# Kernel optimization log

Measured on AMD Instinct MI355X. Metric: run time of the kernel, lower is better.

Reference implementation:

```python
import jax, jax.numpy as jnp
import numpy as np

B, S, D = 8, 1024, 768          # batch, block_size, d_model
H = 6                            # n_head
E = 24                           # n_experts
CAP = 4                          # n_expert_capacity
DH = D // H                      # 128, head dim
DF = 384                         # d_ffn
N = S * H                        # tokens after head split = 6144
K = N * CAP // E                 # tokens per expert = 1024


def _uniform(key, shape, fan_in):
    b = 1.0 / np.sqrt(fan_in)
    return jax.random.uniform(key, shape, jnp.float32, -b, b)


def setup_inputs() -> dict:
    key = jax.random.key(0)
    kx, kc, k1, k2, kh, km = jax.random.split(key, 6)
    return {
        "x": jax.random.normal(kx, (B, S, D), jnp.float32),
        "choice": _uniform(kc, (E, DH), DH),
        "w1": _uniform(k1, (E, DH, DF), DH),
        "w2": _uniform(k2, (E, DF, DH), DF),
        "head": _uniform(kh, (D, D), D),
        "merge": _uniform(km, (D, D), D),
    }


def reference(x, choice, w1, w2, head, merge):
    Bb = x.shape[0]
    # input projection then split heads into a token stream of length N
    x = jnp.einsum("bsd,do->bso", x, head)
    x = x.reshape(Bb, N, DH)                              # [B, N, DH]
    # expert-choice routing: softmax over experts per token
    gates = jax.nn.softmax(jnp.einsum("bsd,ed->bse", x, choice), axis=-1)
    # each expert picks its top-K tokens
    G, I = jax.lax.top_k(jnp.swapaxes(gates, -1, -2), K)  # [B, E, K]
    bidx = jnp.arange(Bb)[:, None, None]
    # gather (equivalent to one-hot matmul einsum('beks,bsd->bekd', P, x))
    x_in = x[bidx, I]                                     # [B, E, K, DH]
    # per-expert SwiGLU-free FFN: silu(x w1) w2
    h = jax.nn.silu(jnp.einsum("bekd,edo->beko", x_in, w1))
    x_mlp = jnp.einsum("beki,eid->bekd", h, w2)           # [B, E, K, DH]
    # scatter-combine weighted by gates (einsum('beks,bek,bekd->bsd'))
    x_out = jnp.zeros((Bb, N, DH), x.dtype).at[bidx, I].add(G[..., None] * x_mlp)
    # dropout is identity in eval mode
    x_out = x_out.reshape(Bb, S, D)
    return jnp.einsum("bsd,do->bso", x_out, merge)
```

## Files before the change

kernel.cpp:

```cpp
#include <hip/hip_runtime.h>
#include <stdint.h>
#include <math.h>

typedef __attribute__((ext_vector_type(8))) short short8;
typedef __attribute__((ext_vector_type(4))) short short4v;
typedef __attribute__((ext_vector_type(4))) float floatx4;
typedef __attribute__((ext_vector_type(2))) float floatx2;
typedef __attribute__((ext_vector_type(4))) double double4v;

#define DEV static __device__ __forceinline__

DEV float bf2f(unsigned short u){ union { unsigned int i; float f; } c; c.i = ((unsigned int)u) << 16; return c.f; }
DEV unsigned short f2bf(float f){ union { float f; unsigned int i; } c; c.f = f; unsigned int u = c.i; u += 0x7fffu + ((u >> 16) & 1u); return (unsigned short)(u >> 16); }

#if defined(__has_builtin)
#if __has_builtin(__builtin_amdgcn_global_load_lds)
#define USE_GLL 1
#endif
#if __has_builtin(__builtin_amdgcn_exp2f) && __has_builtin(__builtin_amdgcn_rcpf)
#define FAST_SILU 1
#endif
#endif
#ifndef USE_GLL
#define USE_GLL 0
#endif
#ifndef FAST_SILU
#define FAST_SILU 0
#endif

DEV void gll16(const unsigned short* g, unsigned short* ldsbase, int lane){
#if USE_GLL
  __builtin_amdgcn_global_load_lds((const __attribute__((address_space(1))) void*)g,
                                   (__attribute__((address_space(3))) void*)ldsbase, 16, 0, 0);
#else
  *(short8*)(ldsbase + lane * 8) = *(const short8*)g;
#endif
}

DEV float silu(float v){
#if FAST_SILU
  float ex = __builtin_amdgcn_exp2f(v * -1.44269504088896f);
  return v * __builtin_amdgcn_rcpf(1.f + ex);
#else
  return v / (1.f + __expf(-v));
#endif
}

DEV void transpose_tile(const float* in, unsigned short* out, int R, int C,
                        int bx, int by, int bz, int tid, unsigned short* tile)
{
  const long boff = (long)bz * (long)R * (long)C;
  in += boff; out += boff;
  const int c0 = bx * 64, r0 = by * 64;
  const int rr = tid >> 4;
  const int c4 = (tid & 15) * 4;
#pragma unroll
  for (int i = 0; i < 4; i++){
    int r = rr + i * 16;
    floatx4 v = *(const floatx4*)(in + (long)(r0 + r) * C + c0 + c4);
#pragma unroll
    for (int u = 0; u < 4; u++) tile[r * 68 + c4 + u] = f2bf(v[u]);
  }
  __syncthreads();
#pragma unroll
  for (int i = 0; i < 4; i++){
    int cc = rr + i * 16;
    short4v v;
#pragma unroll
    for (int u = 0; u < 4; u++) v[u] = (short)tile[(c4 + u) * 68 + cc];
    *(short4v*)(out + (long)(c0 + cc) * R + r0 + c4) = v;
  }
}

__global__ __launch_bounds__(256) void k_prep(const float* __restrict__ x,
    const float* __restrict__ choice, const float* __restrict__ w1,
    const float* __restrict__ w2, const float* __restrict__ head,
    const float* __restrict__ merge,
    unsigned short* __restrict__ xb, unsigned short* __restrict__ headT,
    unsigned short* __restrict__ mergeT, unsigned short* __restrict__ w1T,
    unsigned short* __restrict__ w2T, double* __restrict__ W64,
    unsigned int* __restrict__ probe)
{
  __shared__ double buf[1536];
  unsigned short* tile = (unsigned short*)buf;
  const int id = blockIdx.x, tid = threadIdx.x;
  if (id < 144){
    transpose_tile(head, headT, 768, 768, id % 12, id / 12, 0, tid, tile);
  } else if (id < 288){
    int l = id - 144;
    transpose_tile(merge, mergeT, 768, 768, l % 12, l / 12, 0, tid, tile);
  } else if (id < 576){
    int l = id - 288;
    transpose_tile(w1, w1T, 128, 384, l % 6, (l / 6) % 2, l / 12, tid, tile);
  } else if (id < 864){
    int l = id - 576;
    transpose_tile(w2, w2T, 384, 128, l % 2, (l / 2) % 6, l / 12, tid, tile);
  } else if (id < 1248){
    int l = id - 864;
    const int sub = tid >> 7, lt = tid & 127;
    const int d = l * 2 + sub;
    double* hrow = buf + sub * 768;
    for (int i = lt; i < 768; i += 128) hrow[i] = (double)head[(long)d * 768 + i];
    __syncthreads();
    for (int c = lt; c < 144; c += 128){
      int h = c / 24, e = c % 24;
      double a = 0.0;
      const double* hr = hrow + h * 128;
      const float* ch = choice + e * 128;
#pragma unroll 8
      for (int k = 0; k < 128; k++) a += hr[k] * (double)ch[k];
      W64[(long)d * 144 + c] = a;
    }
  } else if (id < 7392){
    const long l = id - 1248;
    const long i = (l * 256 + tid) * 4;
    floatx4 v = *(const floatx4*)(x + i);
    short4v o;
#pragma unroll
    for (int u = 0; u < 4; u++) o[u] = (short)f2bf(v[u]);
    *(short4v*)(xb + i) = o;
  } else {
    if (tid < 64){
      double4v z = {0.0, 0.0, 0.0, 0.0};
      double4v d1 = __builtin_amdgcn_mfma_f64_16x16x4f64((double)tid, 1.0, z, 0, 0, 0);
      double4v d2 = __builtin_amdgcn_mfma_f64_16x16x4f64(1.0, (double)tid, z, 0, 0, 0);
      const int V0 = (int)d1[0];
      const int Astd = ((V0 & 3) == 0) ? 1 : 0;
      unsigned int rp = 0;
      int V;
      V = (int)d1[0]; rp |= (unsigned int)(Astd ? (V - 96) >> 2 : (V - 6) >> 4);
      V = (int)d1[1]; rp |= (unsigned int)(Astd ? (V - 96) >> 2 : (V - 6) >> 4) << 8;
      V = (int)d1[2]; rp |= (unsigned int)(Astd ? (V - 96) >> 2 : (V - 6) >> 4) << 16;
      V = (int)d1[3]; rp |= (unsigned int)(Astd ? (V - 96) >> 2 : (V - 6) >> 4) << 24;
      const int W0 = (int)d2[0];
      const int Bstd = ((W0 & 3) == 0) ? 1 : 0;
      const int cl = Bstd ? (W0 - 96) >> 2 : (W0 - 6) >> 4;
      probe[tid] = rp;
      probe[64 + tid] = (unsigned int)cl;
      if (tid == 0) probe[128] = (unsigned int)(Astd | (Bstd << 1));
    }
  }
}

template<int OUTF>
DEV void gemm_body(const unsigned short* __restrict__ A, const unsigned short* __restrict__ BT,
                   unsigned short* __restrict__ C, float* __restrict__ Cf, int N, int K,
                   unsigned short* As, unsigned short* Bs, int m0, int n0, int tid)
{
  const int lane = tid & 63;
  const int w = tid >> 6;
  const int wy = w >> 1, wx = w & 1;

  floatx4 acc[4][4];
  {
    floatx4 z4 = {0.f, 0.f, 0.f, 0.f};
#pragma unroll
    for (int i = 0; i < 4; i++)
#pragma unroll
      for (int j = 0; j < 4; j++) acc[i][j] = z4;
  }

  const int rsub = lane >> 3;
  const int kcol = (lane & 7) * 8;

  for (int k0 = 0; k0 < K; k0 += 64){
#pragma unroll
    for (int i = 0; i < 4; i++){
      const int inst = w * 4 + i;
      const int rr = inst * 8 + rsub;
      gll16(A + (long)(m0 + rr) * K + k0 + kcol, &As[inst * 512], lane);
      gll16(BT + (long)(n0 + rr) * K + k0 + kcol, &Bs[inst * 512], lane);
    }
    __syncthreads();
#pragma unroll
    for (int ks = 0; ks < 2; ++ks){
      const int kb = ks * 32 + (lane >> 4) * 8;
      short8 af[4], bfr[4];
#pragma unroll
      for (int mi = 0; mi < 4; mi++) af[mi]  = *(const short8*)&As[(wy * 64 + mi * 16 + (lane & 15)) * 64 + kb];
#pragma unroll
      for (int ni = 0; ni < 4; ni++) bfr[ni] = *(const short8*)&Bs[(wx * 64 + ni * 16 + (lane & 15)) * 64 + kb];
#pragma unroll
      for (int mi = 0; mi < 4; mi++)
#pragma unroll
        for (int ni = 0; ni < 4; ni++)
          acc[mi][ni] = __builtin_amdgcn_mfma_f32_16x16x32_bf16(af[mi], bfr[ni], acc[mi][ni], 0, 0, 0);
    }
    __syncthreads();
  }

  const int ml = lane & 15;
  const int rq = (lane >> 4) * 4;
#pragma unroll
  for (int mi = 0; mi < 4; mi++){
    const int rowb = m0 + wy * 64 + mi * 16 + rq;
#pragma unroll
    for (int ni = 0; ni < 4; ni++){
      const int col = n0 + wx * 64 + ni * 16 + ml;
#pragma unroll
      for (int r = 0; r < 4; r++){
        float v = acc[mi][ni][r];
        if (OUTF) Cf[(long)(rowb + r) * N + col] = v;
        else      C[(long)(rowb + r) * N + col] = f2bf(v);
      }
    }
  }
}

DEV void gates_mfma(const float* __restrict__ xg, const double* __restrict__ W,
                    double* __restrict__ P, const unsigned int* __restrict__ probe,
                    int id, int tid)
{
  const int lane = tid & 63, w = tid >> 6;
  const unsigned int flags = probe[128];
  const int Astd = (int)(flags & 1u), Bstd = (int)((flags >> 1) & 1u);
  const unsigned int rp = probe[lane];
  const int cl = (int)probe[64 + lane];
  const int ar = Astd ? (lane & 15) : (lane >> 2);
  const int ak = Astd ? (lane >> 4) : (lane & 3);
  const int bk = Bstd ? (lane >> 4) : (lane & 3);
  const int bj = Bstd ? (lane & 15) : (lane >> 2);

  const int kseg = id >> 7;
  const int row0 = (id & 127) * 64 + w * 16;

  double4v acc[9];
#pragma unroll
  for (int t = 0; t < 9; t++) acc[t] = (double4v){0.0, 0.0, 0.0, 0.0};

  const float* arow = xg + (long)(row0 + ar) * 768;
  const int kbase = kseg * 192;
  for (int kc = 0; kc < 192; kc += 4){
    const int k0 = kbase + kc;
    const double a = (double)arow[k0 + ak];
    const double* wr = W + (long)(k0 + bk) * 144 + bj;
#pragma unroll
    for (int t = 0; t < 9; t++)
      acc[t] = __builtin_amdgcn_mfma_f64_16x16x4f64(a, wr[t * 16], acc[t], 0, 0, 0);
  }

  const int r0_ = (int)(rp & 255u), r1_ = (int)((rp >> 8) & 255u);
  const int r2_ = (int)((rp >> 16) & 255u), r3_ = (int)((rp >> 24) & 255u);
  double* dst = P + (long)kseg * 8192 * 144 + (long)row0 * 144;
#pragma unroll
  for (int t = 0; t < 9; t++){
    const int cb = t * 16 + cl;
    dst[(long)r0_ * 144 + cb] = acc[t][0];
    dst[(long)r1_ * 144 + cb] = acc[t][1];
    dst[(long)r2_ * 144 + cb] = acc[t][2];
    dst[(long)r3_ * 144 + cb] = acc[t][3];
  }
}

__global__ __launch_bounds__(256, 4) void k_main0(const unsigned short* __restrict__ xb,
    const unsigned short* __restrict__ headT, unsigned short* __restrict__ x1,
    const float* __restrict__ xg, const double* __restrict__ W, double* __restrict__ P,
    const unsigned int* __restrict__ probe)
{
  __shared__ unsigned short lds[128 * 64 * 2];
  const int id = blockIdx.x, tid = threadIdx.x;
  if (id < 512){
    gates_mfma(xg, W, P, probe, id, tid);
  } else {
    const int id2 = id - 512;
    unsigned short* As = lds;
    unsigned short* Bs = As + 128 * 64;
    gemm_body<0>(xb, headT, x1, nullptr, 768, 768, As, Bs, (id2 & 63) * 128, (id2 >> 6) * 128, tid);
  }
}

__global__ __launch_bounds__(256) void k_softmax(const double* __restrict__ P,
                                                 double* __restrict__ gatesT)
{
  const int gid = blockIdx.x * 256 + threadIdx.x;
  const int R = gid / 6, h = gid % 6;
  const int b = R >> 10, s = R & 1023;
  const int n = s * 6 + h;
  const long S = (long)8192 * 144;
  const long base = (long)R * 144 + h * 24;
  double l[24];
#pragma unroll
  for (int e = 0; e < 24; e++){
    const long o = base + e;
    l[e] = (P[o] + P[S + o]) + (P[2 * S + o] + P[3 * S + o]);
  }
  double m = l[0];
#pragma unroll
  for (int e = 1; e < 24; e++) m = fmax(m, l[e]);
  double ssum = 0.0;
#pragma unroll
  for (int e = 0; e < 24; e++){ l[e] = exp(l[e] - m); ssum += l[e]; }
  double is = 1.0 / ssum;
#pragma unroll
  for (int e = 0; e < 24; e++)
    gatesT[((long)(b * 24 + e)) * 6144 + n] = l[e] * is;
}

DEV int blk_reduce(int v, volatile int* sbuf, int tid){
#pragma unroll
  for (int off = 32; off > 0; off >>= 1) v += __shfl_down(v, off);
  __syncthreads();
  if ((tid & 63) == 0) sbuf[tid >> 6] = v;
  __syncthreads();
  return sbuf[0] + sbuf[1] + sbuf[2] + sbuf[3];
}

__global__ __launch_bounds__(256) void k_topk(const double* __restrict__ gatesT,
                                              int* __restrict__ Kidx, float* __restrict__ Gval,
                                              int* __restrict__ cnt, unsigned short* __restrict__ inv)
{
  __shared__ int sbuf[4];
  __shared__ int s_pos;
  __shared__ unsigned long long mm[8];
  const int tid = threadIdx.x;
  const int be = blockIdx.x;
  const int b = be / 24, e = be % 24;
  const double* g = gatesT + (long)be * 6144;

  unsigned long long key[24];
#pragma unroll
  for (int j = 0; j < 24; j++)
    key[j] = (unsigned long long)__double_as_longlong(g[tid + 256 * j]);

  unsigned long long mn = key[0], mx = key[0];
#pragma unroll
  for (int j = 1; j < 24; j++){
    mn = key[j] < mn ? key[j] : mn;
    mx = key[j] > mx ? key[j] : mx;
  }
#pragma unroll
  for (int off = 32; off > 0; off >>= 1){
    unsigned long long a = (unsigned long long)__shfl_down((long long)mn, off);
    unsigned long long c = (unsigned long long)__shfl_down((long long)mx, off);
    mn = a < mn ? a : mn;
    mx = c > mx ? c : mx;
  }
  if ((tid & 63) == 0){ mm[(tid >> 6) * 2] = mn; mm[(tid >> 6) * 2 + 1] = mx; }
  __syncthreads();
  mn = mm[0]; mx = mm[1];
#pragma unroll
  for (int q = 1; q < 4; q++){
    mn = mm[2 * q] < mn ? mm[2 * q] : mn;
    mx = mm[2 * q + 1] > mx ? mm[2 * q + 1] : mx;
  }

  unsigned long long lo = mn - 1ull, hi = mx;
  for (int it = 0; it < 64; ++it){
    if (hi - lo <= 1ull) break;
    unsigned long long mid = lo + ((hi - lo) >> 1);
    int c = 0;
#pragma unroll
    for (int j = 0; j < 24; j++) c += (key[j] > mid) ? 1 : 0;
    c = blk_reduce(c, sbuf, tid);
    if (c >= 1024) lo = mid; else hi = mid;
  }
  const unsigned long long T = hi;
  int cg = 0;
#pragma unroll
  for (int j = 0; j < 24; j++) cg += (key[j] > T) ? 1 : 0;
  cg = blk_reduce(cg, sbuf, tid);
  const int need = 1024 - cg;

  int lo2 = 0, hi2 = 6144;
  for (int it = 0; it < 13; ++it){
    if (hi2 - lo2 <= 1) break;
    int mid = (lo2 + hi2) >> 1;
    int c = 0;
#pragma unroll
    for (int j = 0; j < 24; j++) c += (key[j] == T && (tid + 256 * j) < mid) ? 1 : 0;
    c = blk_reduce(c, sbuf, tid);
    if (c >= need) hi2 = mid; else lo2 = mid;
  }
  const int m = hi2;

  if (tid == 0) s_pos = 0;
  __syncthreads();
#pragma unroll
  for (int j = 0; j < 24; j++){
    int n = tid + 256 * j;
    bool sel = (key[j] > T) || (key[j] == T && n < m);
    if (sel){
      int slot = atomicAdd(&s_pos, 1);
      Kidx[(long)be * 1024 + slot] = n;
      Gval[(long)be * 1024 + slot] = (float)__longlong_as_double((long long)key[j]);
      int t = b * 6144 + n;
      int p = atomicAdd(&cnt[t], 1);
      inv[(long)t * 24 + p] = (unsigned short)(e * 1024 + slot);
    }
  }
}

__global__ __launch_bounds__(256, 2) void k_gemm2(const unsigned short* __restrict__ A,
    const unsigned short* __restrict__ BT, float* __restrict__ Cf)
{
  __shared__ unsigned short As[128 * 64];
  __shared__ unsigned short Bs[128 * 64];
  gemm_body<1>(A, BT, nullptr, Cf, 768, 768, As, Bs,
               (int)blockIdx.x * 128, (int)blockIdx.y * 128, (int)threadIdx.x);
}

__global__ __launch_bounds__(256, 4) void k_ffn(const unsigned short* __restrict__ x1,
    const unsigned short* __restrict__ w1T, const unsigned short* __restrict__ w2T,
    const int* __restrict__ KidxAll, const float* __restrict__ GvalAll,
    unsigned short* __restrict__ Y)
{
  __shared__ unsigned short W1c[64 * 128];
  __shared__ unsigned short W2c[128 * 64];
  __shared__ unsigned short Hc[64 * 64];
  const int tid = threadIdx.x, lane = tid & 63, w = tid >> 6;
  const int tx = lane & 15, quad = lane >> 4;
  const int mt = blockIdx.x;
  const int be = blockIdx.y;
  const int b = be / 24, e = be % 24;
  const int* idx = KidxAll + (long)be * 1024 + mt * 64;
  const float* scl = GvalAll + (long)be * 1024 + mt * 64;
  const unsigned short* A   = x1  + (long)b * 6144 * 128;
  const unsigned short* w1e = w1T + (long)e * 384 * 128;
  const unsigned short* w2e = w2T + (long)e * 128 * 384;

  short8 afr[4];
  {
    const int r0 = idx[w * 16 + tx];
    const unsigned short* a0 = A + (long)r0 * 128 + quad * 8;
#pragma unroll
    for (int ks = 0; ks < 4; ks++) afr[ks] = *(const short8*)(a0 + ks * 32);
  }

  floatx4 Yt[2][4];
  {
    floatx4 z4 = {0.f, 0.f, 0.f, 0.f};
#pragma unroll
    for (int i = 0; i < 2; i++)
#pragma unroll
      for (int j = 0; j < 4; j++) Yt[i][j] = z4;
  }

  for (int nc = 0; nc < 6; ++nc){
    {
      const int r0 = w * 16;
#pragma unroll
      for (int i = 0; i < 4; i++){
        int lr = r0 + i * 4 + quad;
        int c = tx ^ (lr & 15);
        gll16(w1e + (long)(nc * 64 + lr) * 128 + c * 8, &W1c[(r0 + i * 4) * 128], lane);
      }
    }
    {
      const int r0 = w * 32;
#pragma unroll
      for (int i = 0; i < 4; i++){
        int rr = r0 + i * 8 + (lane >> 3);
        int c = (lane & 7) ^ (rr & 7);
        gll16(w2e + (long)rr * 384 + nc * 64 + c * 8, &W2c[(r0 + i * 8) * 64], lane);
      }
    }
    __syncthreads();

    floatx4 h4[4];
    {
      floatx4 z4 = {0.f, 0.f, 0.f, 0.f};
#pragma unroll
      for (int j = 0; j < 4; j++) h4[j] = z4;
    }
#pragma unroll
    for (int ks = 0; ks < 4; ++ks){
      const int chunk = ks * 4 + quad;
      const int pos = chunk ^ tx;
#pragma unroll
      for (int nf = 0; nf < 4; ++nf){
        short8 bfr = *(const short8*)&W1c[(nf * 16 + tx) * 128 + pos * 8];
        h4[nf] = __builtin_amdgcn_mfma_f32_16x16x32_bf16(afr[ks], bfr, h4[nf], 0, 0, 0);
      }
    }
#pragma unroll
    for (int nf = 0; nf < 4; ++nf){
      const int hchunk = nf * 2 + (tx >> 3);
      const int hoff = tx & 7;
#pragma unroll
      for (int r = 0; r < 4; r++){
        float v = silu(h4[nf][r]);
        const int trow = w * 16 + quad * 4 + r;
        Hc[trow * 64 + (hchunk ^ (trow & 7)) * 8 + hoff] = f2bf(v);
      }
    }
    __syncthreads();

#pragma unroll
    for (int ks = 0; ks < 2; ++ks){
      const int chunk2 = ks * 4 + quad;
      const int posx = chunk2 ^ (tx & 7);
      short8 a2[2], b2[4];
#pragma unroll
      for (int mf = 0; mf < 2; ++mf)
        a2[mf] = *(const short8*)&W2c[(w * 32 + mf * 16 + tx) * 64 + posx * 8];
#pragma unroll
      for (int nf = 0; nf < 4; ++nf)
        b2[nf] = *(const short8*)&Hc[(nf * 16 + tx) * 64 + posx * 8];
#pragma unroll
      for (int mf = 0; mf < 2; ++mf)
#pragma unroll
        for (int nf = 0; nf < 4; ++nf)
          Yt[mf][nf] = __builtin_amdgcn_mfma_f32_16x16x32_bf16(a2[mf], b2[nf], Yt[mf][nf], 0, 0, 0);
    }
    __syncthreads();
  }

#pragma unroll
  for (int nf = 0; nf < 4; ++nf){
    const int rb = nf * 16 + tx;
    const float g = scl[rb];
    unsigned short* dst = Y + ((long)be * 1024 + mt * 64 + rb) * 128 + w * 32 + quad * 4;
#pragma unroll
    for (int mf = 0; mf < 2; ++mf){
      short4v v;
#pragma unroll
      for (int r = 0; r < 4; r++) v[r] = (short)f2bf(Yt[mf][nf][r] * g);
      *(short4v*)(dst + mf * 16) = v;
    }
  }
}

__global__ __launch_bounds__(256) void k_combine(const int* __restrict__ cnt,
    const unsigned short* __restrict__ inv, const unsigned short* __restrict__ Y,
    unsigned short* __restrict__ xout)
{
  const int t = blockIdx.x * 4 + (threadIdx.x >> 6);
  const int lane = threadIdx.x & 63;
  const int b = t / 6144;
  const int c = cnt[t];
  float a0 = 0.f, a1 = 0.f;
  for (int p = 0; p < c; ++p){
    int code = inv[(long)t * 24 + p];
    int e = code >> 10, slot = code & 1023;
    const unsigned short* y = Y + (((long)(b * 24 + e) * 1024 + slot) << 7) + lane * 2;
    a0 += bf2f(y[0]); a1 += bf2f(y[1]);
  }
  unsigned short* o = xout + ((long)t << 7) + lane * 2;
  o[0] = f2bf(a0); o[1] = f2bf(a1);
}

extern "C" void kernel_launch(void* const* d_in, const int* in_sizes, int n_in,
                              void* d_out, int out_size, void* d_ws, size_t ws_size,
                              hipStream_t stream)
{
  const float* x      = (const float*)d_in[0];
  const float* choice = (const float*)d_in[1];
  const float* w1     = (const float*)d_in[2];
  const float* w2     = (const float*)d_in[3];
  const float* head   = (const float*)d_in[4];
  const float* merge  = (const float*)d_in[5];
  float* out = (float*)d_out;
  (void)in_sizes; (void)n_in; (void)out_size; (void)ws_size;

  char* p = (char*)d_ws;
  auto alloc = [&p](size_t bytes) -> void* {
    void* q = (void*)p; p += (bytes + 255) & ~(size_t)255; return q;
  };

  unsigned short* headT = (unsigned short*)alloc((size_t)768 * 768 * 2);
  unsigned short* mergeT= (unsigned short*)alloc((size_t)768 * 768 * 2);
  unsigned short* w1T   = (unsigned short*)alloc((size_t)24 * 384 * 128 * 2);
  unsigned short* w2T   = (unsigned short*)alloc((size_t)24 * 128 * 384 * 2);
  double* W64           = (double*)alloc((size_t)768 * 144 * 8);
  int* Kidx             = (int*)alloc((size_t)192 * 1024 * 4);
  float* Gval           = (float*)alloc((size_t)192 * 1024 * 4);
  int* cnt              = (int*)alloc((size_t)49152 * 4);
  unsigned short* inv   = (unsigned short*)alloc((size_t)49152 * 24 * 2);
  unsigned short* xb    = (unsigned short*)alloc((size_t)8192 * 768 * 2);
  unsigned short* x1    = (unsigned short*)alloc((size_t)8192 * 768 * 2);
  unsigned short* Y     = (unsigned short*)alloc((size_t)192 * 1024 * 128 * 2);
  double* P             = (double*)Y;
  double* gatesT        = (double*)((char*)Y + (size_t)4 * 8192 * 144 * 8);
  unsigned short* xout  = xb;
  unsigned int* probe   = (unsigned int*)Kidx;

  hipMemsetAsync(cnt, 0, (size_t)49152 * 4, stream);
  k_prep<<<dim3(7393), 256, 0, stream>>>(x, choice, w1, w2, head, merge,
                                         xb, headT, mergeT, w1T, w2T, W64, probe);
  k_main0<<<dim3(896), 256, 0, stream>>>(xb, headT, x1, x, W64, P, probe);
  k_softmax<<<dim3(192), 256, 0, stream>>>(P, gatesT);
  k_topk<<<dim3(192), 256, 0, stream>>>(gatesT, Kidx, Gval, cnt, inv);
  k_ffn<<<dim3(16, 192, 1), 256, 0, stream>>>(x1, w1T, w2T, Kidx, Gval, Y);
  k_combine<<<dim3(12288), 256, 0, stream>>>(cnt, inv, Y, xout);
  k_gemm2<<<dim3(64, 6, 1), 256, 0, stream>>>(xout, mergeT, out);
}
```

Baseline: 335.6 us.

## Halve gate k-split, single-barrier topk reduction, batch combine gathers

Gate-logit MFMA work is split into two k-segments of 384 instead of four of 192, so fewer partial buffers are written and summed in softmax. The block reduction in top-k uses a double-buffered shared array so each step needs one barrier instead of two. The combine kernel loads four inverse-index codes at once and issues four independent 32-bit gathers per iteration to raise memory-level parallelism. The gates split trades parallelism (fewer blocks, longer per-block loops) for less partial-sum traffic.

```diff
diff --git a/kernel.cpp b/kernel.cpp
--- a/kernel.cpp
+++ b/kernel.cpp
@@ -229,8 +229,8 @@
   for (int t = 0; t < 9; t++) acc[t] = (double4v){0.0, 0.0, 0.0, 0.0};
 
   const float* arow = xg + (long)(row0 + ar) * 768;
-  const int kbase = kseg * 192;
-  for (int kc = 0; kc < 192; kc += 4){
+  const int kbase = kseg * 384;
+  for (int kc = 0; kc < 384; kc += 4){
     const int k0 = kbase + kc;
     const double a = (double)arow[k0 + ak];
     const double* wr = W + (long)(k0 + bk) * 144 + bj;
@@ -259,10 +259,10 @@
 {
   __shared__ unsigned short lds[128 * 64 * 2];
   const int id = blockIdx.x, tid = threadIdx.x;
-  if (id < 512){
+  if (id < 256){
     gates_mfma(xg, W, P, probe, id, tid);
   } else {
-    const int id2 = id - 512;
+    const int id2 = id - 256;
     unsigned short* As = lds;
     unsigned short* Bs = As + 128 * 64;
     gemm_body<0>(xb, headT, x1, nullptr, 768, 768, As, Bs, (id2 & 63) * 128, (id2 >> 6) * 128, tid);
@@ -282,7 +282,7 @@
 #pragma unroll
   for (int e = 0; e < 24; e++){
     const long o = base + e;
-    l[e] = (P[o] + P[S + o]) + (P[2 * S + o] + P[3 * S + o]);
+    l[e] = P[o] + P[S + o];
   }
   double m = l[0];
 #pragma unroll
@@ -296,26 +296,27 @@
     gatesT[((long)(b * 24 + e)) * 6144 + n] = l[e] * is;
 }
 
-DEV int blk_reduce(int v, volatile int* sbuf, int tid){
+DEV int blk_reduce(int v, volatile int* sbuf, int tid, int ph){
 #pragma unroll
   for (int off = 32; off > 0; off >>= 1) v += __shfl_down(v, off);
+  volatile int* sb = sbuf + (ph & 1) * 4;
+  if ((tid & 63) == 0) sb[tid >> 6] = v;
   __syncthreads();
-  if ((tid & 63) == 0) sbuf[tid >> 6] = v;
-  __syncthreads();
-  return sbuf[0] + sbuf[1] + sbuf[2] + sbuf[3];
+  return sb[0] + sb[1] + sb[2] + sb[3];
 }
 
 __global__ __launch_bounds__(256) void k_topk(const double* __restrict__ gatesT,
                                               int* __restrict__ Kidx, float* __restrict__ Gval,
                                               int* __restrict__ cnt, unsigned short* __restrict__ inv)
 {
-  __shared__ int sbuf[4];
+  __shared__ int sbuf[8];
   __shared__ int s_pos;
   __shared__ unsigned long long mm[8];
   const int tid = threadIdx.x;
   const int be = blockIdx.x;
   const int b = be / 24, e = be % 24;
   const double* g = gatesT + (long)be * 6144;
+  int ph = 0;
 
   unsigned long long key[24];
 #pragma unroll
@@ -351,14 +352,14 @@
     int c = 0;
 #pragma unroll
     for (int j = 0; j < 24; j++) c += (key[j] > mid) ? 1 : 0;
-    c = blk_reduce(c, sbuf, tid);
+    c = blk_reduce(c, sbuf, tid, ph++);
     if (c >= 1024) lo = mid; else hi = mid;
   }
   const unsigned long long T = hi;
   int cg = 0;
 #pragma unroll
   for (int j = 0; j < 24; j++) cg += (key[j] > T) ? 1 : 0;
-  cg = blk_reduce(cg, sbuf, tid);
+  cg = blk_reduce(cg, sbuf, tid, ph++);
   const int need = 1024 - cg;
 
   int lo2 = 0, hi2 = 6144;
@@ -368,7 +369,7 @@
     int c = 0;
 #pragma unroll
     for (int j = 0; j < 24; j++) c += (key[j] == T && (tid + 256 * j) < mid) ? 1 : 0;
-    c = blk_reduce(c, sbuf, tid);
+    c = blk_reduce(c, sbuf, tid, ph++);
     if (c >= need) hi2 = mid; else lo2 = mid;
   }
   const int m = hi2;
@@ -528,12 +529,27 @@
   const int lane = threadIdx.x & 63;
   const int b = t / 6144;
   const int c = cnt[t];
+  const unsigned short* ivp = inv + (long)t * 24;
+  const unsigned short* Yb = Y + ((long)(b * 24) << 17);
   float a0 = 0.f, a1 = 0.f;
-  for (int p = 0; p < c; ++p){
-    int code = inv[(long)t * 24 + p];
-    int e = code >> 10, slot = code & 1023;
-    const unsigned short* y = Y + (((long)(b * 24 + e) * 1024 + slot) << 7) + lane * 2;
-    a0 += bf2f(y[0]); a1 += bf2f(y[1]);
+  int p = 0;
+  for (; p + 4 <= c; p += 4){
+    unsigned long long iv = *(const unsigned long long*)(ivp + p);
+    const int c0 = (int)(iv & 0xffffu), c1 = (int)((iv >> 16) & 0xffffu);
+    const int c2 = (int)((iv >> 32) & 0xffffu), c3 = (int)(iv >> 48);
+    unsigned int v0 = *(const unsigned int*)(Yb + (((long)c0) << 7) + lane * 2);
+    unsigned int v1 = *(const unsigned int*)(Yb + (((long)c1) << 7) + lane * 2);
+    unsigned int v2 = *(const unsigned int*)(Yb + (((long)c2) << 7) + lane * 2);
+    unsigned int v3 = *(const unsigned int*)(Yb + (((long)c3) << 7) + lane * 2);
+    a0 += bf2f((unsigned short)v0); a1 += bf2f((unsigned short)(v0 >> 16));
+    a0 += bf2f((unsigned short)v1); a1 += bf2f((unsigned short)(v1 >> 16));
+    a0 += bf2f((unsigned short)v2); a1 += bf2f((unsigned short)(v2 >> 16));
+    a0 += bf2f((unsigned short)v3); a1 += bf2f((unsigned short)(v3 >> 16));
+  }
+  for (; p < c; ++p){
+    const int code = ivp[p];
+    unsigned int v = *(const unsigned int*)(Yb + (((long)code) << 7) + lane * 2);
+    a0 += bf2f((unsigned short)v); a1 += bf2f((unsigned short)(v >> 16));
   }
   unsigned short* o = xout + ((long)t << 7) + lane * 2;
   o[0] = f2bf(a0); o[1] = f2bf(a1);
@@ -570,14 +586,14 @@
   unsigned short* x1    = (unsigned short*)alloc((size_t)8192 * 768 * 2);
   unsigned short* Y     = (unsigned short*)alloc((size_t)192 * 1024 * 128 * 2);
   double* P             = (double*)Y;
-  double* gatesT        = (double*)((char*)Y + (size_t)4 * 8192 * 144 * 8);
+  double* gatesT        = (double*)((char*)Y + (size_t)2 * 8192 * 144 * 8);
   unsigned short* xout  = xb;
   unsigned int* probe   = (unsigned int*)Kidx;
 
   hipMemsetAsync(cnt, 0, (size_t)49152 * 4, stream);
   k_prep<<<dim3(7393), 256, 0, stream>>>(x, choice, w1, w2, head, merge,
                                          xb, headT, mergeT, w1T, w2T, W64, probe);
-  k_main0<<<dim3(896), 256, 0, stream>>>(xb, headT, x1, x, W64, P, probe);
+  k_main0<<<dim3(640), 256, 0, stream>>>(xb, headT, x1, x, W64, P, probe);
   k_softmax<<<dim3(192), 256, 0, stream>>>(P, gatesT);
   k_topk<<<dim3(192), 256, 0, stream>>>(gatesT, Kidx, Gval, cnt, inv);
   k_ffn<<<dim3(16, 192, 1), 256, 0, stream>>>(x1, w1T, w2T, Kidx, Gval, Y);
```

Result: slower. 349.5 us (+4.1%).
